# Optimization experiments

Hardware: AMD Instinct MI355X
Metric: run time of the kernel (lower is better)

The kernel has to match this reference:

```python
import jax, jax.numpy as jnp
import numpy as np

N_CLASSES = 4096
FEAT_DIM = 2048


def setup_inputs() -> dict:
    key = jax.random.key(0)
    k1, k2, k3 = jax.random.split(key, 3)
    boundaries = jax.random.uniform(k1, (N_CLASSES,), dtype=jnp.float32)
    prototypes = jax.random.normal(k2, (N_CLASSES, FEAT_DIM), dtype=jnp.float32)
    classifier_weights = jax.random.normal(k3, (N_CLASSES, FEAT_DIM), dtype=jnp.float32)
    return {"boundaries": boundaries, "prototypes": prototypes,
            "classifier_weights": classifier_weights}


def reference(boundaries, prototypes, classifier_weights):
    n = boundaries.shape[0]
    # L2-normalize prototypes along feature dim (F.normalize, eps=1e-12)
    norm = jnp.sqrt(jnp.sum(prototypes * prototypes, axis=-1, keepdims=True))
    p = prototypes / jnp.maximum(norm, 1e-12)
    # s[i, j] = <p_i, w_j>  -- one GEMM instead of N^2 tiny dots
    s = p @ classifier_weights.T  # [N, N]
    diag = jnp.diagonal(s)  # <p_i, w_i>, shape [N]
    # term1 depends only on i, term2 on (i, j)
    term1 = (1.0 - boundaries) * diag  # [N]
    term2 = s * (boundaries - 1.0)[None, :]  # [N, N], broadcast over j
    vals = jax.nn.relu(term1[:, None] + term2)  # [N, N]
    # exclude i == j
    off_diag_sum = jnp.sum(vals) - jnp.sum(jnp.diagonal(vals))
    return off_diag_sum / (n * (n - 1))
```

## Files before the change

kernel.cpp:

```cpp
#include <hip/hip_runtime.h>
#include <hip/hip_bf16.h>

#define N_CLS 4096
#define FDIM  2048
#define NT    16

typedef float  floatx4 __attribute__((ext_vector_type(4)));
typedef int    intx2   __attribute__((ext_vector_type(2)));
typedef int    intx4   __attribute__((ext_vector_type(4)));
typedef int    intx8   __attribute__((ext_vector_type(8)));

__global__ __launch_bounds__(256) void prep_kernel(
    const float* __restrict__ bnd,
    const float* __restrict__ proto,
    const float* __restrict__ wgt,
    unsigned char* __restrict__ pf8,
    unsigned char* __restrict__ wf8,
    float* __restrict__ t1,
    float* __restrict__ cc,
    float* __restrict__ accum)
{
    const int row = blockIdx.x;
    const int tid = threadIdx.x;
    const size_t base = (size_t)row * FDIM + (size_t)tid * 8;

    floatx4 p0 = *(const floatx4*)(proto + base);
    floatx4 p1 = *(const floatx4*)(proto + base + 4);
    floatx4 w0 = *(const floatx4*)(wgt + base);
    floatx4 w1 = *(const floatx4*)(wgt + base + 4);

    float ss = 0.f, dt = 0.f;
#pragma unroll
    for (int k = 0; k < 4; ++k) {
        ss += p0[k] * p0[k] + p1[k] * p1[k];
        dt += p0[k] * w0[k] + p1[k] * w1[k];
    }
#pragma unroll
    for (int off = 32; off > 0; off >>= 1) {
        ss += __shfl_down(ss, off);
        dt += __shfl_down(dt, off);
    }

    __shared__ float sss[4], sdt[4];
    __shared__ float srn;
    const int wid = tid >> 6, lane = tid & 63;
    if (lane == 0) { sss[wid] = ss; sdt[wid] = dt; }
    __syncthreads();
    if (tid == 0) {
        float SS = sss[0] + sss[1] + sss[2] + sss[3];
        float DT = sdt[0] + sdt[1] + sdt[2] + sdt[3];
        float rn = 1.0f / fmaxf(sqrtf(SS), 1e-12f);
        srn = rn;
        float bv = bnd[row];
        t1[row] = (1.0f - bv) * (DT * rn);
        cc[row] = bv - 1.0f;
        if (row == 0) *accum = 0.0f;
    }
    __syncthreads();
    const float rn = srn;

    intx2 pv, wv;
    {
        int a = __builtin_amdgcn_cvt_pk_fp8_f32(p0[0] * rn, p0[1] * rn, 0, 0);
        a     = __builtin_amdgcn_cvt_pk_fp8_f32(p0[2] * rn, p0[3] * rn, a, 1);
        int b = __builtin_amdgcn_cvt_pk_fp8_f32(p1[0] * rn, p1[1] * rn, 0, 0);
        b     = __builtin_amdgcn_cvt_pk_fp8_f32(p1[2] * rn, p1[3] * rn, b, 1);
        pv[0] = a; pv[1] = b;
        int c = __builtin_amdgcn_cvt_pk_fp8_f32(w0[0], w0[1], 0, 0);
        c     = __builtin_amdgcn_cvt_pk_fp8_f32(w0[2], w0[3], c, 1);
        int d = __builtin_amdgcn_cvt_pk_fp8_f32(w1[0], w1[1], 0, 0);
        d     = __builtin_amdgcn_cvt_pk_fp8_f32(w1[2], w1[3], d, 1);
        wv[0] = c; wv[1] = d;
    }
    *(intx2*)(pf8 + base) = pv;
    *(intx2*)(wf8 + base) = wv;
}

#define PH_BAR() { __builtin_amdgcn_s_barrier(); __builtin_amdgcn_sched_barrier(0); }
#define VMCNT(N) asm volatile("s_waitcnt vmcnt(" #N ")" ::: "memory")

#define RD_FA(D, MH)                                                           \
    _Pragma("unroll") for (int mi = 0; mi < 4; ++mi) {                         \
        const unsigned char* bp = &sAB[D][aoff + ((MH)*64 + mi*16) * 128];     \
        intx4* fp = (intx4*)&fa[mi];                                           \
        fp[0] = *(const intx4*)(bp + cq0);                                     \
        fp[1] = *(const intx4*)(bp + cq1);                                     \
    }
#define RD_FB2(D, NI0)                                                         \
    _Pragma("unroll") for (int ni = 0; ni < 2; ++ni) {                         \
        const unsigned char* bp = &sAB[D][boff + ((NI0)+ni) * 2048];           \
        intx4* fp = (intx4*)&fb[(NI0)+ni];                                     \
        fp[0] = *(const intx4*)(bp + cq0);                                     \
        fp[1] = *(const intx4*)(bp + cq1);                                     \
    }
#define MFMA_Q(MI0, NI0)                                                       \
    __builtin_amdgcn_s_setprio(1);                                             \
    _Pragma("unroll") for (int mi = 0; mi < 4; ++mi)                           \
    _Pragma("unroll") for (int ni = 0; ni < 2; ++ni)                           \
        acc[(MI0)+mi][(NI0)+ni] =                                              \
            __builtin_amdgcn_mfma_scale_f32_16x16x128_f8f6f4(                  \
                fa[mi], fb[(NI0)+ni], acc[(MI0)+mi][(NI0)+ni],                 \
                0, 0, 0, SC1, 0, SC1);                                         \
    __builtin_amdgcn_s_setprio(0);

__global__ __launch_bounds__(512, 1) void gemm_reduce_kernel(
    const unsigned char* __restrict__ A,
    const unsigned char* __restrict__ B,
    const float* __restrict__ t1,
    const float* __restrict__ cc,
    float* __restrict__ accum)
{
    __shared__ unsigned char sAB[2][65536];
    __shared__ float red[8];

    const int tid  = threadIdx.x;
    const int wid  = tid >> 6;
    const int lane = tid & 63;
    const int SC1  = 0x7F7F7F7F;

    const int b   = blockIdx.x;
    const int xcd = b & 7, sl = b >> 3;
    const int bi  = ((xcd & 3) << 2) + (sl & 3);
    const int bj  = ((xcd >> 2) << 3) + (sl >> 2);
    const int arow0 = bi * 256;
    const int brow0 = bj * 256;

    const int wm = wid >> 2;
    const int wn = wid & 3;
    const int lr = lane & 15;
    const int q  = lane >> 4;
    const int r7 = lane & 7;

    const int cq0 = ((q)     ^ r7) << 4;
    const int cq1 = ((4 | q) ^ r7) << 4;
    const int aoff = wm * 16384 + lr * 128;
    const int boff = 32768 + (wn >> 1) * 16384 + (wn & 1) * 8192 + lr * 128;

    const int srow = tid >> 3;
    const int sx   = (tid & 7) ^ ((tid >> 3) & 7);
    const int sgc  = (((sx & 3) << 1) | (sx >> 2)) << 4;

    auto glds = [&](const unsigned char* src, unsigned char* dst) {
        __builtin_amdgcn_global_load_lds(
            (const __attribute__((address_space(1))) void*)src,
            (__attribute__((address_space(3))) void*)dst, 16, 0, 0);
    };
    auto stageA = [&](int h, int t) {
        unsigned char* dst = &sAB[t & 1][h * 16384 + tid * 16];
        const unsigned char* src =
            A + (size_t)(arow0 + h * 128 + srow) * FDIM + t * 128 + sgc;
        glds(src, dst);
        glds(src + (size_t)64 * FDIM, dst + 8192);
    };
    auto stageB = [&](int h, int t) {
        unsigned char* dst = &sAB[t & 1][32768 + h * 16384 + tid * 16];
        const unsigned char* src =
            B + (size_t)(brow0 + h * 128 + srow) * FDIM + t * 128 + sgc;
        glds(src, dst);
        glds(src + (size_t)64 * FDIM, dst + 8192);
    };

    floatx4 acc[8][4];
#pragma unroll
    for (int m = 0; m < 8; ++m)
#pragma unroll
        for (int n = 0; n < 4; ++n) acc[m][n] = (floatx4)0.0f;

    intx8 fa[4];
    intx8 fb[4];

    stageA(0, 0); stageA(1, 0); stageB(0, 0); stageB(1, 0);

#pragma unroll 1
    for (int t = 0; t < NT; ++t) {
        const int D = t & 1;

        VMCNT(0);
        PH_BAR();

        if (t + 1 < NT) {
            stageA(0, t + 1); stageA(1, t + 1);
            stageB(0, t + 1); stageB(1, t + 1);
        }

        RD_FA(D, 0);
        RD_FB2(D, 0); RD_FB2(D, 2);
        MFMA_Q(0, 0); MFMA_Q(0, 2);
        RD_FA(D, 1);
        MFMA_Q(4, 0); MFMA_Q(4, 2);
    }

    const int row0 = arow0 + wm * 128 + (lane >> 4) * 4;
    const int col0 = brow0 + wn * 64 + lr;

    float local = 0.f;
#pragma unroll
    for (int n = 0; n < 4; ++n) {
        const int j = col0 + n * 16;
        const float cj = cc[j];
#pragma unroll
        for (int m = 0; m < 8; ++m) {
#pragma unroll
            for (int r = 0; r < 4; ++r) {
                const int i = row0 + m * 16 + r;
                float v = fmaxf(t1[i] + acc[m][n][r] * cj, 0.f);
                local += (i == j) ? 0.f : v;
            }
        }
    }

#pragma unroll
    for (int off = 32; off > 0; off >>= 1)
        local += __shfl_down(local, off);
    if (lane == 0) red[wid] = local;
    __syncthreads();
    if (tid == 0) {
        float s = 0.f;
#pragma unroll
        for (int w = 0; w < 8; ++w) s += red[w];
        atomicAdd(accum, s);
    }
}

__global__ void finalize_kernel(const float* __restrict__ accum,
                                float* __restrict__ out)
{
    const float denom = 4096.0f * 4095.0f;
    out[0] = *accum / denom;
}

extern "C" void kernel_launch(void* const* d_in, const int* in_sizes, int n_in,
                              void* d_out, int out_size, void* d_ws, size_t ws_size,
                              hipStream_t stream) {
    const float* bnd   = (const float*)d_in[0];
    const float* proto = (const float*)d_in[1];
    const float* wgt   = (const float*)d_in[2];

    char* ws = (char*)d_ws;
    unsigned char* pf8 = (unsigned char*)ws;
    unsigned char* wf8 = (unsigned char*)(ws + (size_t)N_CLS * FDIM);
    float* t1    = (float*)(ws + (size_t)N_CLS * FDIM * 2);
    float* cc    = t1 + N_CLS;
    float* accum = cc + N_CLS;

    prep_kernel<<<N_CLS, 256, 0, stream>>>(bnd, proto, wgt, pf8, wf8, t1, cc, accum);
    gemm_reduce_kernel<<<256, 512, 0, stream>>>(pf8, wf8, t1, cc, accum);
    finalize_kernel<<<1, 1, 0, stream>>>(accum, (float*)d_out);
}
```

Baseline: 53.42 us.

## Load B fragments directly from global into registers, bypassing LDS staging

Drops LDS staging for the B operand and halves shared memory to hold only A tiles. Each wave now loads its B MFMA fragments straight from global memory at the top of each K step. This removes the LDS writes and reads for B and frees shared memory. In exchange, global latency sits on the critical path because there is no prefetch, and waves that share the same B columns load them twice.

```diff
diff --git a/kernel.cpp b/kernel.cpp
--- a/kernel.cpp
+++ b/kernel.cpp
@@ -81,17 +81,18 @@
 
 #define RD_FA(D, MH)                                                           \
     _Pragma("unroll") for (int mi = 0; mi < 4; ++mi) {                         \
-        const unsigned char* bp = &sAB[D][aoff + ((MH)*64 + mi*16) * 128];     \
+        const unsigned char* bp = &sA[D][aoff + ((MH)*64 + mi*16) * 128];      \
         intx4* fp = (intx4*)&fa[mi];                                           \
         fp[0] = *(const intx4*)(bp + cq0);                                     \
         fp[1] = *(const intx4*)(bp + cq1);                                     \
     }
-#define RD_FB2(D, NI0)                                                         \
+#define LD_FB2(NI0, T)                                                         \
     _Pragma("unroll") for (int ni = 0; ni < 2; ++ni) {                         \
-        const unsigned char* bp = &sAB[D][boff + ((NI0)+ni) * 2048];           \
+        const unsigned char* gp = Bbase + (size_t)(((NI0)+ni) * 16) * FDIM     \
+                                  + (T) * 128;                                 \
         intx4* fp = (intx4*)&fb[(NI0)+ni];                                     \
-        fp[0] = *(const intx4*)(bp + cq0);                                     \
-        fp[1] = *(const intx4*)(bp + cq1);                                     \
+        fp[0] = *(const intx4*)(gp);                                           \
+        fp[1] = *(const intx4*)(gp + 16);                                      \
     }
 #define MFMA_Q(MI0, NI0)                                                       \
     __builtin_amdgcn_s_setprio(1);                                             \
@@ -110,7 +111,7 @@
     const float* __restrict__ cc,
     float* __restrict__ accum)
 {
-    __shared__ unsigned char sAB[2][65536];
+    __shared__ unsigned char sA[2][32768];
     __shared__ float red[8];
 
     const int tid  = threadIdx.x;
@@ -134,7 +135,9 @@
     const int cq0 = ((q)     ^ r7) << 4;
     const int cq1 = ((4 | q) ^ r7) << 4;
     const int aoff = wm * 16384 + lr * 128;
-    const int boff = 32768 + (wn >> 1) * 16384 + (wn & 1) * 8192 + lr * 128;
+
+    const unsigned char* Bbase =
+        B + (size_t)(brow0 + wn * 64 + lr) * FDIM + q * 32;
 
     const int srow = tid >> 3;
     const int sx   = (tid & 7) ^ ((tid >> 3) & 7);
@@ -146,19 +149,12 @@
             (__attribute__((address_space(3))) void*)dst, 16, 0, 0);
     };
     auto stageA = [&](int h, int t) {
-        unsigned char* dst = &sAB[t & 1][h * 16384 + tid * 16];
+        unsigned char* dst = &sA[t & 1][h * 16384 + tid * 16];
         const unsigned char* src =
             A + (size_t)(arow0 + h * 128 + srow) * FDIM + t * 128 + sgc;
         glds(src, dst);
         glds(src + (size_t)64 * FDIM, dst + 8192);
     };
-    auto stageB = [&](int h, int t) {
-        unsigned char* dst = &sAB[t & 1][32768 + h * 16384 + tid * 16];
-        const unsigned char* src =
-            B + (size_t)(brow0 + h * 128 + srow) * FDIM + t * 128 + sgc;
-        glds(src, dst);
-        glds(src + (size_t)64 * FDIM, dst + 8192);
-    };
 
     floatx4 acc[8][4];
 #pragma unroll
@@ -169,7 +165,7 @@
     intx8 fa[4];
     intx8 fb[4];
 
-    stageA(0, 0); stageA(1, 0); stageB(0, 0); stageB(1, 0);
+    stageA(0, 0); stageA(1, 0);
 
 #pragma unroll 1
     for (int t = 0; t < NT; ++t) {
@@ -178,13 +174,10 @@
         VMCNT(0);
         PH_BAR();
 
-        if (t + 1 < NT) {
-            stageA(0, t + 1); stageA(1, t + 1);
-            stageB(0, t + 1); stageB(1, t + 1);
-        }
-
+        if (t + 1 < NT) { stageA(0, t + 1); stageA(1, t + 1); }
+
+        LD_FB2(0, t); LD_FB2(2, t);
         RD_FA(D, 0);
-        RD_FB2(D, 0); RD_FB2(D, 2);
         MFMA_Q(0, 0); MFMA_Q(0, 2);
         RD_FA(D, 1);
         MFMA_Q(4, 0); MFMA_Q(4, 2);
```

After: 70.32 us. +31.6%, slower.
